# Kernel optimization log

Measured on AMD Instinct MI355X. Metric: run time of the kernel, lower is better.

## Reference

```python
import jax, jax.numpy as jnp
import numpy as np

WINDOW = 20
EPS = 1e-08


def setup_inputs() -> dict:
    key = jax.random.key(0)
    k1, _ = jax.random.split(key)
    B, F, T = 16, 257, 8000
    mag = jax.random.uniform(k1, (B, F, T), dtype=jnp.float32)  # magnitudes are nonnegative
    bias = jnp.zeros((1,), dtype=jnp.float32)
    return {"mag": mag, "bias": bias}


def reference(mag, bias):
    # mag: [B, F, T]; causal sliding-window mean over (F, last WINDOW frames).
    B, F, T = mag.shape
    frame_sum = mag.sum(axis=1)  # [B, T] sum over frequency
    # exclusive-prefix-padded cumsum along time -> O(T) windowed sums
    cs = jnp.concatenate([jnp.zeros((B, 1), mag.dtype), jnp.cumsum(frame_sum, axis=1)], axis=1)  # [B, T+1]
    t = jnp.arange(T)
    start = jnp.maximum(0, t - WINDOW + 1)                 # causal clamp at sequence start
    count = ((t - start + 1) * F).astype(mag.dtype)        # valid elements per window
    win_sum = cs[:, t + 1] - cs[:, start]                  # [B, T]
    mean = win_sum / count + bias                          # learnable bias, broadcast [1]
    mean = mean[:, None, :]                                # [B, 1, T]
    norm = mag / (mean + EPS)                              # [B, F, T]
    return norm, mean
```

## Files before the change

### kernel.cpp

```cpp
#include <hip/hip_runtime.h>

#define WINDOW 20
#define EPS 1e-8f

constexpr int B = 16;
constexpr int F = 257;
constexpr int T = 8000;
constexpr int TQ = T / 4;
constexpr int CHUNK_Q = 32;
constexpr int NCH = 2;
constexpr int TILE_Q = CHUNK_Q * NCH;
constexpr int NTILES = (TQ + TILE_Q - 1) / TILE_Q;

typedef float f32x4 __attribute__((ext_vector_type(4)));

__device__ __forceinline__ void bar_lds() {
  asm volatile("s_waitcnt lgkmcnt(0)" ::: "memory");
  __builtin_amdgcn_s_barrier();
}

__device__ __forceinline__ void nt_store4(float4* p, float4 v) {
  f32x4 w = {v.x, v.y, v.z, v.w};
  __builtin_nontemporal_store(w, (f32x4*)p);
}

__global__ void __launch_bounds__(512) fused_kernel(
    const float* __restrict__ mag, const float* __restrict__ bias,
    float* __restrict__ out_norm, float* __restrict__ out_mean) {

  const int b    = blockIdx.y;
  const int q0   = blockIdx.x * TILE_Q;
  const int tid  = threadIdx.x;
  const int q    = tid & (CHUNK_Q - 1);
  const int rg   = tid >> 5;
  const int wave = tid >> 6;
  const int lane = tid & 63;

  const float4* magq = (const float4*)(mag + (size_t)b * F * T);
  float4* outq = (float4*)(out_norm + (size_t)b * F * T);
  const float bs = bias[0];

  __shared__ float4 red[16][CHUNK_Q];
  __shared__ float  cs[20 + CHUNK_Q * 4];
  __shared__ float4 inv4[CHUNK_Q];

  if (wave < 5) {
    int qh = q0 - 5 + wave;
    float4 hs = make_float4(0.f, 0.f, 0.f, 0.f);
    if (qh >= 0) {
      #pragma unroll
      for (int r = 0; r < 4; ++r) {
        float4 tv = magq[(size_t)(lane + (r << 6)) * TQ + qh];
        hs.x += tv.x; hs.y += tv.y; hs.z += tv.z; hs.w += tv.w;
      }
      if (lane == 0) {
        float4 tv = magq[(size_t)256 * TQ + qh];
        hs.x += tv.x; hs.y += tv.y; hs.z += tv.z; hs.w += tv.w;
      }
    }
    #pragma unroll
    for (int off = 32; off > 0; off >>= 1) {
      hs.x += __shfl_down(hs.x, off);
      hs.y += __shfl_down(hs.y, off);
      hs.z += __shfl_down(hs.z, off);
      hs.w += __shfl_down(hs.w, off);
    }
    if (lane == 0) {
      cs[4 * wave + 0] = hs.x;
      cs[4 * wave + 1] = hs.y;
      cs[4 * wave + 2] = hs.z;
      cs[4 * wave + 3] = hs.w;
    }
  }

  for (int ch = 0; ch < NCH; ++ch) {
    const int cq0 = q0 + ch * CHUNK_Q;
    if (cq0 >= TQ) break;
    const int qc  = min(CHUNK_Q, TQ - cq0);
    const bool act = (q < qc);

    float4 v[16];
    float4 v16 = make_float4(0.f, 0.f, 0.f, 0.f);
    float4 acc = make_float4(0.f, 0.f, 0.f, 0.f);
    if (act) {
      const float4* p = magq + cq0 + q;
      #pragma unroll
      for (int it = 0; it < 16; ++it) {
        float4 tv = p[(size_t)((it << 4) + rg) * TQ];
        v[it] = tv;
        acc.x += tv.x; acc.y += tv.y; acc.z += tv.z; acc.w += tv.w;
      }
      if (rg == 0) {
        v16 = p[(size_t)256 * TQ];
        acc.x += v16.x; acc.y += v16.y; acc.z += v16.z; acc.w += v16.w;
      }
    }
    red[rg][q] = acc;
    bar_lds();

    if (tid < CHUNK_Q) {
      float4 s = make_float4(0.f, 0.f, 0.f, 0.f);
      #pragma unroll
      for (int r = 0; r < 16; ++r) {
        float4 a = red[r][tid];
        s.x += a.x; s.y += a.y; s.z += a.z; s.w += a.w;
      }
      cs[20 + 4 * tid + 0] = s.x;
      cs[20 + 4 * tid + 1] = s.y;
      cs[20 + 4 * tid + 2] = s.z;
      cs[20 + 4 * tid + 3] = s.w;
    }
    bar_lds();

    const int ncols = qc * 4;
    if (tid < ncols) {
      int t = cq0 * 4 + tid;
      float ws = 0.f;
      #pragma unroll
      for (int k = 0; k < WINDOW; ++k) ws += cs[20 + tid - k];
      int nwin = (t < WINDOW - 1) ? (t + 1) : WINDOW;
      float mean = ws / (float)(nwin * F) + bs;
      out_mean[b * T + t] = mean;
      ((float*)inv4)[tid] = 1.0f / (mean + EPS);
    }
    bar_lds();

    if (act) {
      float4 w = inv4[q];
      float4* o = outq + cq0 + q;
      #pragma unroll
      for (int it = 0; it < 16; ++it) {
        float4 tv = v[it];
        tv.x *= w.x; tv.y *= w.y; tv.z *= w.z; tv.w *= w.w;
        nt_store4(&o[(size_t)((it << 4) + rg) * TQ], tv);
      }
      if (rg == 0) {
        float4 tv = v16;
        tv.x *= w.x; tv.y *= w.y; tv.z *= w.z; tv.w *= w.w;
        nt_store4(&o[(size_t)256 * TQ], tv);
      }
    }
    if (tid < 20) cs[tid] = cs[ncols + tid];
  }
}

extern "C" void kernel_launch(void* const* d_in, const int* in_sizes, int n_in,
                              void* d_out, int out_size, void* d_ws, size_t ws_size,
                              hipStream_t stream) {
  const float* mag  = (const float*)d_in[0];
  const float* bias = (const float*)d_in[1];
  float* out_norm = (float*)d_out;
  float* out_mean = (float*)d_out + (size_t)B * F * T;

  dim3 grid(NTILES, B);
  fused_kernel<<<grid, 512, 0, stream>>>(mag, bias, out_norm, out_mean);
}
```

Baseline: 49.51 us.

## Process one chunk per block and merge reduction and window-mean phases

Each block now handles a single 32-quad chunk instead of two sequential chunks, doubling the grid and dropping the carried halo state. The main tile loads are issued before the halo reduction so those loads overlap it. The column reduction and windowed-mean computation now run inside wave 0 with only a wave-local LDS wait, which removes one block-wide barrier. Each lane computes two adjacent means using an incremental window update. The trade-off is that every block recomputes its 5-quad halo, adding redundant halo reads.

```diff
diff --git a/kernel.cpp b/kernel.cpp
--- a/kernel.cpp
+++ b/kernel.cpp
@@ -8,9 +8,7 @@
 constexpr int T = 8000;
 constexpr int TQ = T / 4;
 constexpr int CHUNK_Q = 32;
-constexpr int NCH = 2;
-constexpr int TILE_Q = CHUNK_Q * NCH;
-constexpr int NTILES = (TQ + TILE_Q - 1) / TILE_Q;
+constexpr int NTILES = (TQ + CHUNK_Q - 1) / CHUNK_Q;
 
 typedef float f32x4 __attribute__((ext_vector_type(4)));
 
@@ -29,7 +27,7 @@
     float* __restrict__ out_norm, float* __restrict__ out_mean) {
 
   const int b    = blockIdx.y;
-  const int q0   = blockIdx.x * TILE_Q;
+  const int q0   = blockIdx.x * CHUNK_Q;
   const int tid  = threadIdx.x;
   const int q    = tid & (CHUNK_Q - 1);
   const int rg   = tid >> 5;
@@ -43,6 +41,26 @@
   __shared__ float4 red[16][CHUNK_Q];
   __shared__ float  cs[20 + CHUNK_Q * 4];
   __shared__ float4 inv4[CHUNK_Q];
+
+  const int qc  = min(CHUNK_Q, TQ - q0);
+  const bool act = (q < qc);
+
+  float4 v[16];
+  float4 v16 = make_float4(0.f, 0.f, 0.f, 0.f);
+  float4 acc = make_float4(0.f, 0.f, 0.f, 0.f);
+  if (act) {
+    const float4* p = magq + q0 + q;
+    #pragma unroll
+    for (int it = 0; it < 16; ++it) {
+      float4 tv = p[(size_t)((it << 4) + rg) * TQ];
+      v[it] = tv;
+      acc.x += tv.x; acc.y += tv.y; acc.z += tv.z; acc.w += tv.w;
+    }
+    if (rg == 0) {
+      v16 = p[(size_t)256 * TQ];
+      acc.x += v16.x; acc.y += v16.y; acc.z += v16.z; acc.w += v16.w;
+    }
+  }
 
   if (wave < 5) {
     int qh = q0 - 5 + wave;
@@ -73,74 +91,57 @@
     }
   }
 
-  for (int ch = 0; ch < NCH; ++ch) {
-    const int cq0 = q0 + ch * CHUNK_Q;
-    if (cq0 >= TQ) break;
-    const int qc  = min(CHUNK_Q, TQ - cq0);
-    const bool act = (q < qc);
+  red[rg][q] = acc;
+  bar_lds();
 
-    float4 v[16];
-    float4 v16 = make_float4(0.f, 0.f, 0.f, 0.f);
-    float4 acc = make_float4(0.f, 0.f, 0.f, 0.f);
-    if (act) {
-      const float4* p = magq + cq0 + q;
-      #pragma unroll
-      for (int it = 0; it < 16; ++it) {
-        float4 tv = p[(size_t)((it << 4) + rg) * TQ];
-        v[it] = tv;
-        acc.x += tv.x; acc.y += tv.y; acc.z += tv.z; acc.w += tv.w;
-      }
-      if (rg == 0) {
-        v16 = p[(size_t)256 * TQ];
-        acc.x += v16.x; acc.y += v16.y; acc.z += v16.z; acc.w += v16.w;
-      }
-    }
-    red[rg][q] = acc;
-    bar_lds();
-
-    if (tid < CHUNK_Q) {
+  if (wave == 0) {
+    if (lane < CHUNK_Q) {
       float4 s = make_float4(0.f, 0.f, 0.f, 0.f);
       #pragma unroll
       for (int r = 0; r < 16; ++r) {
-        float4 a = red[r][tid];
+        float4 a = red[r][lane];
         s.x += a.x; s.y += a.y; s.z += a.z; s.w += a.w;
       }
-      cs[20 + 4 * tid + 0] = s.x;
-      cs[20 + 4 * tid + 1] = s.y;
-      cs[20 + 4 * tid + 2] = s.z;
-      cs[20 + 4 * tid + 3] = s.w;
+      ((float4*)(cs + 20))[lane] = s;
     }
-    bar_lds();
-
+    asm volatile("s_waitcnt lgkmcnt(0)" ::: "memory");
     const int ncols = qc * 4;
-    if (tid < ncols) {
-      int t = cq0 * 4 + tid;
+    int c = lane * 2;
+    if (c < ncols) {
+      int t = q0 * 4 + c;
       float ws = 0.f;
       #pragma unroll
-      for (int k = 0; k < WINDOW; ++k) ws += cs[20 + tid - k];
+      for (int k = 0; k < WINDOW; ++k) ws += cs[20 + c - k];
       int nwin = (t < WINDOW - 1) ? (t + 1) : WINDOW;
       float mean = ws / (float)(nwin * F) + bs;
       out_mean[b * T + t] = mean;
-      ((float*)inv4)[tid] = 1.0f / (mean + EPS);
+      ((float*)inv4)[c] = 1.0f / (mean + EPS);
+
+      int c1 = c + 1;
+      float ws1 = ws + cs[20 + c1] - cs[c1];
+      int t1 = t + 1;
+      int nwin1 = (t1 < WINDOW - 1) ? (t1 + 1) : WINDOW;
+      float mean1 = ws1 / (float)(nwin1 * F) + bs;
+      out_mean[b * T + t1] = mean1;
+      ((float*)inv4)[c1] = 1.0f / (mean1 + EPS);
     }
-    bar_lds();
+  }
+  bar_lds();
 
-    if (act) {
-      float4 w = inv4[q];
-      float4* o = outq + cq0 + q;
-      #pragma unroll
-      for (int it = 0; it < 16; ++it) {
-        float4 tv = v[it];
-        tv.x *= w.x; tv.y *= w.y; tv.z *= w.z; tv.w *= w.w;
-        nt_store4(&o[(size_t)((it << 4) + rg) * TQ], tv);
-      }
-      if (rg == 0) {
-        float4 tv = v16;
-        tv.x *= w.x; tv.y *= w.y; tv.z *= w.z; tv.w *= w.w;
-        nt_store4(&o[(size_t)256 * TQ], tv);
-      }
+  if (act) {
+    float4 w = inv4[q];
+    float4* o = outq + q0 + q;
+    #pragma unroll
+    for (int it = 0; it < 16; ++it) {
+      float4 tv = v[it];
+      tv.x *= w.x; tv.y *= w.y; tv.z *= w.z; tv.w *= w.w;
+      nt_store4(&o[(size_t)((it << 4) + rg) * TQ], tv);
     }
-    if (tid < 20) cs[tid] = cs[ncols + tid];
+    if (rg == 0) {
+      float4 tv = v16;
+      tv.x *= w.x; tv.y *= w.y; tv.z *= w.z; tv.w *= w.w;
+      nt_store4(&o[(size_t)256 * TQ], tv);
+    }
   }
 }
 
```

Result: no change. 49.41 us (-0.2%).
